# Kernel optimization log

Measured on AMD Instinct MI355X. Metric: run time of the kernel, lower is better.

Reference implementation:

```python
import jax, jax.numpy as jnp
import numpy as np

EPS = 1e-5
LEAK = 0.33  # scn LeakyReLU default leakiness


def leaky(x):
    return jnp.where(x > 0, x, LEAK * x)


def subm_conv(feat, idx, mask, w):
    # feat: [N,C], idx: [N,K] int, mask: [N,K] bool, w: [K,Cin,Cout]
    g = feat[idx] * mask[..., None]          # [N,K,C] gather of active neighbors
    return jnp.einsum('nkc,kcd->nd', g, w)   # [N,Cout]


def batch_norm(x, gamma, beta):
    # scn BatchNormalization in training mode: batch stats over active sites
    m = x.mean(axis=0)
    v = x.var(axis=0)
    return (x - m) * jax.lax.rsqrt(v + EPS) * gamma + beta


def setup_inputs() -> dict:
    key = jax.random.key(0)
    ks = jax.random.split(key, 8)
    N, K, C, B = 131072, 9, 64, 4
    features = jax.random.normal(ks[0], (N, C), dtype=jnp.float32)
    neighbor_idx = jax.random.randint(ks[1], (N, K), 0, N, dtype=jnp.int32)
    # center offset always points at self (submanifold conv semantics)
    neighbor_idx = neighbor_idx.at[:, K // 2].set(jnp.arange(N, dtype=jnp.int32))
    neighbor_mask = jax.random.randint(ks[2], (N, K), 0, 2) > 0
    neighbor_mask = neighbor_mask.at[:, K // 2].set(True)
    scale = 1.0 / np.sqrt(K * C)
    conv1_w = jax.random.normal(ks[3], (B, K, C, C), dtype=jnp.float32) * scale
    conv2_w = jax.random.normal(ks[4], (B, K, C, C), dtype=jnp.float32) * scale
    bn1_gamma = jnp.ones((B, C), dtype=jnp.float32)
    bn1_beta = jnp.zeros((B, C), dtype=jnp.float32)
    bn2_gamma = jnp.ones((B, C), dtype=jnp.float32)
    bn2_beta = jnp.zeros((B, C), dtype=jnp.float32)
    return {
        'features': features, 'neighbor_idx': neighbor_idx, 'neighbor_mask': neighbor_mask,
        'conv1_w': conv1_w, 'bn1_gamma': bn1_gamma, 'bn1_beta': bn1_beta,
        'conv2_w': conv2_w, 'bn2_gamma': bn2_gamma, 'bn2_beta': bn2_beta,
    }


def reference(features, neighbor_idx, neighbor_mask, conv1_w, bn1_gamma, bn1_beta,
              conv2_w, bn2_gamma, bn2_beta):
    x = features
    n_blocks = conv1_w.shape[0]
    for b in range(n_blocks):
        residual = x
        out = subm_conv(x, neighbor_idx, neighbor_mask, conv1_w[b])
        out = leaky(batch_norm(out, bn1_gamma[b], bn1_beta[b]))
        out = subm_conv(out, neighbor_idx, neighbor_mask, conv2_w[b])
        out = batch_norm(out, bn2_gamma[b], bn2_beta[b])
        x = leaky(out + residual)
    return x
```

## Files before the change

kernel.cpp:

```cpp
#include <hip/hip_runtime.h>
#include <hip/hip_bf16.h>
#include <stdint.h>

#define NROWS 131072
#define EPSBN 1e-5f
#define LEAKK 0.33f

typedef __bf16 bf16x8_t __attribute__((ext_vector_type(8)));
typedef float  f32x4_t  __attribute__((ext_vector_type(4)));

__device__ __forceinline__ float leaky_f(float x) { return fmaxf(x, LEAKK * x); }

#define GLDS16(g, l)                                                          \
    __builtin_amdgcn_global_load_lds(                                         \
        (const __attribute__((address_space(1))) void*)(g),                   \
        (__attribute__((address_space(3))) void*)(l), 16, 0, 0)

#define CFENCE() asm volatile("" ::: "memory")

__global__ __launch_bounds__(256, 2) void conv_kernel(
    const __bf16* __restrict__ src,
    const int* __restrict__ cidxT,
    const __bf16* __restrict__ wt,
    __bf16* __restrict__ dst,
    float* __restrict__ stat_out)
{
    __shared__ char Bw[9][8192];

    const int tid  = threadIdx.x;
    const int lane = tid & 63;
    const int wv   = tid >> 6;
    const int quad = lane >> 4;
    const int l15  = lane & 15;
    const int row0 = blockIdx.x << 8;
    const int srow = tid >> 3;
    const int cg   = (tid & 7) ^ (srow & 7);
    const int ldsl = (tid & 192) << 4;
    const int sxor = l15 & 7;

    const char* srcb = (const char*)src;
    const char* wtb  = (const char*)wt;

    f32x4_t acc[4][4];
#pragma unroll
    for (int mt = 0; mt < 4; ++mt)
#pragma unroll
        for (int nt = 0; nt < 4; ++nt)
            acc[mt][nt] = (f32x4_t){0.f, 0.f, 0.f, 0.f};

    const int ibase = row0 + (wv << 6) + l15;
    const unsigned qofs = (unsigned)(quad << 4);

    int ixv[2][4];
#pragma unroll
    for (int mt = 0; mt < 4; ++mt) ixv[0][mt] = cidxT[ibase + (mt << 4)];
#pragma unroll
    for (int mt = 0; mt < 4; ++mt) ixv[1][mt] = cidxT[NROWS + ibase + (mt << 4)];
    CFENCE();
#pragma unroll
    for (int k = 0; k < 9; ++k)
#pragma unroll
        for (int i = 0; i < 2; ++i)
            GLDS16(wtb + (k << 13) + (((i << 5) + srow) << 7) + (cg << 4),
                   &Bw[k][(i << 12) + ldsl]);
    CFENCE();
    asm volatile("s_waitcnt vmcnt(0)" ::: "memory");
    __builtin_amdgcn_s_barrier();
    CFENCE();

    bf16x8_t areg[2][4][2];
#pragma unroll
    for (int mt = 0; mt < 4; ++mt) {
        unsigned vo = ((unsigned)ixv[0][mt] << 7) + qofs;
#pragma unroll
        for (int ks = 0; ks < 2; ++ks)
            areg[0][mt][ks] = *(const bf16x8_t*)(srcb + vo + (ks << 6));
    }
    CFENCE();

#pragma unroll
    for (int k = 0; k < 9; ++k) {
        if (k < 7) {
#pragma unroll
            for (int mt = 0; mt < 4; ++mt)
                ixv[k & 1][mt] = cidxT[(k + 2) * NROWS + ibase + (mt << 4)];
        }
        if (k < 8) {
#pragma unroll
            for (int mt = 0; mt < 4; ++mt) {
                unsigned vo = ((unsigned)ixv[(k + 1) & 1][mt] << 7) + qofs;
#pragma unroll
                for (int ks = 0; ks < 2; ++ks)
                    areg[(k + 1) & 1][mt][ks] =
                        *(const bf16x8_t*)(srcb + vo + (ks << 6));
            }
        }
        CFENCE();
        bf16x8_t bq[4][2];
#pragma unroll
        for (int ks = 0; ks < 2; ++ks) {
            const int slot = ((quad | (ks << 2)) ^ sxor) << 4;
#pragma unroll
            for (int nt = 0; nt < 4; ++nt)
                bq[nt][ks] = *(const bf16x8_t*)
                    &Bw[k][(((nt << 4) + l15) << 7) + slot];
        }
#pragma unroll
        for (int ks = 0; ks < 2; ++ks)
#pragma unroll
            for (int mt = 0; mt < 4; ++mt)
#pragma unroll
                for (int nt = 0; nt < 4; ++nt)
                    acc[mt][nt] = __builtin_amdgcn_mfma_f32_16x16x32_bf16(
                        areg[k & 1][mt][ks], bq[nt][ks], acc[mt][nt], 0, 0, 0);
        CFENCE();
    }

#pragma unroll
    for (int mt = 0; mt < 4; ++mt) {
        int rowb = row0 + (wv << 6) + (mt << 4) + (quad << 2);
#pragma unroll
        for (int nt = 0; nt < 4; ++nt) {
            int col = (nt << 4) + l15;
#pragma unroll
            for (int r = 0; r < 4; ++r)
                dst[((size_t)(rowb + r) << 6) + col] = (__bf16)acc[mt][nt][r];
        }
    }
    float* red = (float*)Bw;
    __syncthreads();
    if (tid < 128) red[tid] = 0.f;
    __syncthreads();
#pragma unroll
    for (int nt = 0; nt < 4; ++nt) {
        float s = 0.f, q = 0.f;
#pragma unroll
        for (int mt = 0; mt < 4; ++mt)
#pragma unroll
            for (int r = 0; r < 4; ++r) { float v = acc[mt][nt][r]; s += v; q += v * v; }
        s += __shfl_xor(s, 16); s += __shfl_xor(s, 32);
        q += __shfl_xor(q, 16); q += __shfl_xor(q, 32);
        if (lane < 16) {
            atomicAdd(&red[(nt << 4) + lane], s);
            atomicAdd(&red[64 + (nt << 4) + lane], q);
        }
    }
    __syncthreads();
    if (tid < 128) atomicAdd(&stat_out[tid], red[tid]);
}

__global__ __launch_bounds__(256) void bnact_kernel(
    __bf16* __restrict__ y, const float* __restrict__ stat,
    const float* __restrict__ gamma, const float* __restrict__ beta)
{
    __shared__ float sc[64], sh[64];
    int tid = threadIdx.x;
    if (tid < 64) {
        float m = stat[tid] * (1.f / NROWS);
        float v = stat[64 + tid] * (1.f / NROWS) - m * m;
        float s = gamma[tid] * rsqrtf(v + EPSBN);
        sc[tid] = s;
        sh[tid] = beta[tid] - m * s;
    }
    __syncthreads();
    size_t base = ((((size_t)blockIdx.x << 8) | tid) << 3);
    int c0 = (int)(base & 63);
    bf16x8_t hv = *(bf16x8_t*)(y + base);
#pragma unroll
    for (int j = 0; j < 8; ++j) {
        float f = (float)hv[j];
        f = leaky_f(f * sc[c0 + j] + sh[c0 + j]);
        hv[j] = (__bf16)f;
    }
    *(bf16x8_t*)(y + base) = hv;
}

__global__ __launch_bounds__(256) void resid_kernel(
    const __bf16* __restrict__ z, const float* __restrict__ featin,
    __bf16* __restrict__ xh, float* __restrict__ dout,
    const float* __restrict__ stat, const float* __restrict__ gamma,
    const float* __restrict__ beta, int isfirst, int isfinal)
{
    __shared__ float sc[64], sh[64];
    int tid = threadIdx.x;
    if (tid < 64) {
        float m = stat[tid] * (1.f / NROWS);
        float v = stat[64 + tid] * (1.f / NROWS) - m * m;
        float s = gamma[tid] * rsqrtf(v + EPSBN);
        sc[tid] = s;
        sh[tid] = beta[tid] - m * s;
    }
    __syncthreads();
    size_t base = ((((size_t)blockIdx.x << 8) | tid) << 3);
    int c0 = (int)(base & 63);
    bf16x8_t zv = *(const bf16x8_t*)(z + base);
    float xv[8];
    if (isfirst) {
        float4 xa = *(const float4*)(featin + base);
        float4 xb = *(const float4*)(featin + base + 4);
#pragma unroll
        for (int j = 0; j < 4; ++j) { xv[j] = (&xa.x)[j]; xv[4 + j] = (&xb.x)[j]; }
    } else {
        bf16x8_t xr = *(const bf16x8_t*)(xh + base);
#pragma unroll
        for (int j = 0; j < 8; ++j) xv[j] = (float)xr[j];
    }
    float o[8];
#pragma unroll
    for (int j = 0; j < 8; ++j)
        o[j] = leaky_f((float)zv[j] * sc[c0 + j] + sh[c0 + j] + xv[j]);
    if (isfinal) {
        *(float4*)(dout + base)     = make_float4(o[0], o[1], o[2], o[3]);
        *(float4*)(dout + base + 4) = make_float4(o[4], o[5], o[6], o[7]);
    } else {
        bf16x8_t h;
#pragma unroll
        for (int j = 0; j < 8; ++j) h[j] = (__bf16)o[j];
        *(bf16x8_t*)(xh + base) = h;
    }
}

__global__ __launch_bounds__(256) void prep_kernel(
    const float* __restrict__ feat, const float* __restrict__ w1,
    const float* __restrict__ w2, const int* __restrict__ nidx,
    const unsigned char* __restrict__ mraw,
    __bf16* __restrict__ fh, __bf16* __restrict__ yh,
    __bf16* __restrict__ wtp, int* __restrict__ cidxT,
    float* __restrict__ stats)
{
    size_t t = ((size_t)blockIdx.x << 8) | threadIdx.x;
    if (t < 1024) stats[t] = 0.f;
    if (t < 64) {
        fh[(size_t)NROWS * 64 + t] = (__bf16)0.f;
        yh[(size_t)NROWS * 64 + t] = (__bf16)0.f;
    }
    if (t < 1048576) {
        size_t i = t << 3;
        float4 a = *(const float4*)(feat + i);
        float4 b = *(const float4*)(feat + i + 4);
        bf16x8_t h;
        h[0] = (__bf16)a.x; h[1] = (__bf16)a.y; h[2] = (__bf16)a.z; h[3] = (__bf16)a.w;
        h[4] = (__bf16)b.x; h[5] = (__bf16)b.y; h[6] = (__bf16)b.z; h[7] = (__bf16)b.w;
        *(bf16x8_t*)(fh + i) = h;
    }
    if (t < 294912) {
        int o = (int)t;
        int c = o & 63, d = (o >> 6) & 63;
        int kk = o >> 12;
        int k = kk % 9, bb = (kk / 9) & 3, cv = kk / 36;
        const float* w = cv ? w2 : w1;
        float v = w[((size_t)((bb * 9 + k) * 64 + c) << 6) + d];
        wtp[o] = (__bf16)v;
    }
    if (t < NROWS) {
        int n = (int)t;
        bool benc = (mraw[13] != 0);
        const unsigned int* mw = (const unsigned int*)mraw;
#pragma unroll
        for (int j = 0; j < 9; ++j) {
            int e = n * 9 + j;
            bool m = benc ? (mraw[e] != 0) : (mw[e] != 0u);
            cidxT[j * NROWS + n] = m ? nidx[e] : NROWS;
        }
    }
}

extern "C" void kernel_launch(void* const* d_in, const int* in_sizes, int n_in,
                              void* d_out, int out_size, void* d_ws, size_t ws_size,
                              hipStream_t stream) {
    const float* feat = (const float*)d_in[0];
    const int* nidx = (const int*)d_in[1];
    const unsigned char* mraw = (const unsigned char*)d_in[2];
    const float* w1 = (const float*)d_in[3];
    const float* g1 = (const float*)d_in[4];
    const float* b1 = (const float*)d_in[5];
    const float* w2 = (const float*)d_in[6];
    const float* g2 = (const float*)d_in[7];
    const float* b2 = (const float*)d_in[8];
    float* out = (float*)d_out;

    char* ws = (char*)d_ws;
    __bf16* xh    = (__bf16*)ws;
    __bf16* yh    = (__bf16*)(ws + 17825792);
    __bf16* zh    = (__bf16*)(ws + 35651584);
    __bf16* wtp   = (__bf16*)(ws + 53477376);
    float*  stats = (float*)(ws + 54525952);
    int*    cidxT = (int*)(ws + 54591488);

    prep_kernel<<<4096, 256, 0, stream>>>(feat, w1, w2, nidx, mraw,
                                          xh, yh, wtp, cidxT, stats);

    for (int b = 0; b < 4; ++b) {
        conv_kernel<<<512, 256, 0, stream>>>(
            xh, cidxT, wtp + (size_t)b * 9 * 4096,
            yh, stats + (size_t)(2 * b) * 128);
        bnact_kernel<<<4096, 256, 0, stream>>>(
            yh, stats + (size_t)(2 * b) * 128, g1 + b * 64, b1 + b * 64);
        conv_kernel<<<512, 256, 0, stream>>>(
            yh, cidxT, wtp + (size_t)(4 + b) * 9 * 4096,
            zh, stats + (size_t)(2 * b + 1) * 128);
        resid_kernel<<<4096, 256, 0, stream>>>(
            zh, feat, xh, out,
            stats + (size_t)(2 * b + 1) * 128, g2 + b * 64, b2 + b * 64,
            (b == 0) ? 1 : 0, (b == 3) ? 1 : 0);
    }
}
```

Baseline: 404.2 us.

## Fuse batch-norm, activation and residual into conv via a grid-wide barrier

The separate bnact and resid elementwise kernels are removed. Each conv launch now runs a fixed 256-block grid of 512 threads that accumulates BN statistics, waits at a software grid barrier (an atomic counter plus spin), and then applies normalisation, LeakyReLU and the optional residual directly to the accumulators before writing. This drops the intermediate bf16 tensor round-trips and half of the kernel launches per block. The gather prefetch is deepened to three stages and MFMA issue priority is raised with setprio. The barrier relies on all 256 blocks being co-resident and has a bounded spin that would silently give wrong stats on timeout.

```diff
diff --git a/kernel.cpp b/kernel.cpp
--- a/kernel.cpp
+++ b/kernel.cpp
@@ -5,6 +5,7 @@
 #define NROWS 131072
 #define EPSBN 1e-5f
 #define LEAKK 0.33f
+#define NBLK  256
 
 typedef __bf16 bf16x8_t __attribute__((ext_vector_type(8)));
 typedef float  f32x4_t  __attribute__((ext_vector_type(4)));
@@ -18,12 +19,15 @@
 
 #define CFENCE() asm volatile("" ::: "memory")
 
-__global__ __launch_bounds__(256, 2) void conv_kernel(
+__global__ __launch_bounds__(512, 1) void conv_kernel(
     const __bf16* __restrict__ src,
     const int* __restrict__ cidxT,
     const __bf16* __restrict__ wt,
-    __bf16* __restrict__ dst,
-    float* __restrict__ stat_out)
+    __bf16* dst,
+    float* __restrict__ stat,
+    const float* __restrict__ gamma, const float* __restrict__ beta,
+    const __bf16* residh, const float* residf,
+    float* dout, int mode)
 {
     __shared__ char Bw[9][8192];
 
@@ -32,10 +36,10 @@
     const int wv   = tid >> 6;
     const int quad = lane >> 4;
     const int l15  = lane & 15;
-    const int row0 = blockIdx.x << 8;
+    const int row0 = blockIdx.x << 9;
     const int srow = tid >> 3;
     const int cg   = (tid & 7) ^ (srow & 7);
-    const int ldsl = (tid & 192) << 4;
+    const int ldsl = (tid & 448) << 4;
     const int sxor = l15 & 7;
 
     const char* srcb = (const char*)src;
@@ -51,47 +55,49 @@
     const int ibase = row0 + (wv << 6) + l15;
     const unsigned qofs = (unsigned)(quad << 4);
 
-    int ixv[2][4];
-#pragma unroll
-    for (int mt = 0; mt < 4; ++mt) ixv[0][mt] = cidxT[ibase + (mt << 4)];
-#pragma unroll
-    for (int mt = 0; mt < 4; ++mt) ixv[1][mt] = cidxT[NROWS + ibase + (mt << 4)];
+#pragma unroll
+    for (int k = 0; k < 9; ++k)
+        GLDS16(wtb + (k << 13) + (srow << 7) + (cg << 4), &Bw[k][ldsl]);
     CFENCE();
-#pragma unroll
-    for (int k = 0; k < 9; ++k)
-#pragma unroll
-        for (int i = 0; i < 2; ++i)
-            GLDS16(wtb + (k << 13) + (((i << 5) + srow) << 7) + (cg << 4),
-                   &Bw[k][(i << 12) + ldsl]);
+    int ixv[3][4];
+#pragma unroll
+    for (int kk = 0; kk < 3; ++kk)
+#pragma unroll
+        for (int mt = 0; mt < 4; ++mt)
+            ixv[kk][mt] = cidxT[kk * NROWS + ibase + (mt << 4)];
     CFENCE();
-    asm volatile("s_waitcnt vmcnt(0)" ::: "memory");
+    asm volatile("s_waitcnt vmcnt(12)" ::: "memory");
     __builtin_amdgcn_s_barrier();
     CFENCE();
 
-    bf16x8_t areg[2][4][2];
-#pragma unroll
-    for (int mt = 0; mt < 4; ++mt) {
-        unsigned vo = ((unsigned)ixv[0][mt] << 7) + qofs;
-#pragma unroll
-        for (int ks = 0; ks < 2; ++ks)
-            areg[0][mt][ks] = *(const bf16x8_t*)(srcb + vo + (ks << 6));
-    }
-    CFENCE();
+    bf16x8_t areg[3][4][2];
+#pragma unroll
+    for (int kk = 0; kk < 2; ++kk) {
+#pragma unroll
+        for (int mt = 0; mt < 4; ++mt) {
+            unsigned vo = ((unsigned)ixv[kk][mt] << 7) + qofs;
+#pragma unroll
+            for (int ks = 0; ks < 2; ++ks)
+                areg[kk][mt][ks] = *(const bf16x8_t*)(srcb + vo + (ks << 6));
+        }
+        CFENCE();
+    }
 
 #pragma unroll
     for (int k = 0; k < 9; ++k) {
+        if (k < 6) {
+#pragma unroll
+            for (int mt = 0; mt < 4; ++mt)
+                ixv[k % 3][mt] = cidxT[(k + 3) * NROWS + ibase + (mt << 4)];
+        }
+        CFENCE();
         if (k < 7) {
 #pragma unroll
-            for (int mt = 0; mt < 4; ++mt)
-                ixv[k & 1][mt] = cidxT[(k + 2) * NROWS + ibase + (mt << 4)];
-        }
-        if (k < 8) {
-#pragma unroll
             for (int mt = 0; mt < 4; ++mt) {
-                unsigned vo = ((unsigned)ixv[(k + 1) & 1][mt] << 7) + qofs;
+                unsigned vo = ((unsigned)ixv[(k + 2) % 3][mt] << 7) + qofs;
 #pragma unroll
                 for (int ks = 0; ks < 2; ++ks)
-                    areg[(k + 1) & 1][mt][ks] =
+                    areg[(k + 2) % 3][mt][ks] =
                         *(const bf16x8_t*)(srcb + vo + (ks << 6));
             }
         }
@@ -105,6 +111,7 @@
                 bq[nt][ks] = *(const bf16x8_t*)
                     &Bw[k][(((nt << 4) + l15) << 7) + slot];
         }
+        __builtin_amdgcn_s_setprio(1);
 #pragma unroll
         for (int ks = 0; ks < 2; ++ks)
 #pragma unroll
@@ -112,22 +119,14 @@
 #pragma unroll
                 for (int nt = 0; nt < 4; ++nt)
                     acc[mt][nt] = __builtin_amdgcn_mfma_f32_16x16x32_bf16(
-                        areg[k & 1][mt][ks], bq[nt][ks], acc[mt][nt], 0, 0, 0);
-        CFENCE();
-    }
-
-#pragma unroll
-    for (int mt = 0; mt < 4; ++mt) {
-        int rowb = row0 + (wv << 6) + (mt << 4) + (quad << 2);
-#pragma unroll
-        for (int nt = 0; nt < 4; ++nt) {
-            int col = (nt << 4) + l15;
-#pragma unroll
-            for (int r = 0; r < 4; ++r)
-                dst[((size_t)(rowb + r) << 6) + col] = (__bf16)acc[mt][nt][r];
-        }
-    }
+                        areg[k % 3][mt][ks], bq[nt][ks], acc[mt][nt], 0, 0, 0);
+        __builtin_amdgcn_s_setprio(0);
+        CFENCE();
+    }
+
     float* red = (float*)Bw;
+    float* sc  = red + 128;
+    float* sh  = red + 192;
     __syncthreads();
     if (tid < 128) red[tid] = 0.f;
     __syncthreads();
@@ -146,77 +145,54 @@
         }
     }
     __syncthreads();
-    if (tid < 128) atomicAdd(&stat_out[tid], red[tid]);
-}
-
-__global__ __launch_bounds__(256) void bnact_kernel(
-    __bf16* __restrict__ y, const float* __restrict__ stat,
-    const float* __restrict__ gamma, const float* __restrict__ beta)
-{
-    __shared__ float sc[64], sh[64];
-    int tid = threadIdx.x;
+    if (tid < 128) atomicAdd(&stat[tid], red[tid]);
+    __threadfence();
+    __syncthreads();
+
+    int* cnt = (int*)(stat + 128);
+    if (tid == 0) {
+        __hip_atomic_fetch_add(cnt, 1, __ATOMIC_ACQ_REL, __HIP_MEMORY_SCOPE_AGENT);
+        int it = 0;
+        while (__hip_atomic_load(cnt, __ATOMIC_ACQUIRE, __HIP_MEMORY_SCOPE_AGENT)
+                   < NBLK && it < (1 << 20)) {
+            __builtin_amdgcn_s_sleep(2);
+            ++it;
+        }
+    }
+    __syncthreads();
+    __threadfence();
+
     if (tid < 64) {
-        float m = stat[tid] * (1.f / NROWS);
-        float v = stat[64 + tid] * (1.f / NROWS) - m * m;
+        float sm = __hip_atomic_load(&stat[tid],      __ATOMIC_ACQUIRE,
+                                     __HIP_MEMORY_SCOPE_AGENT);
+        float sq = __hip_atomic_load(&stat[64 + tid], __ATOMIC_ACQUIRE,
+                                     __HIP_MEMORY_SCOPE_AGENT);
+        float m = sm * (1.f / NROWS);
+        float v = sq * (1.f / NROWS) - m * m;
         float s = gamma[tid] * rsqrtf(v + EPSBN);
         sc[tid] = s;
         sh[tid] = beta[tid] - m * s;
     }
     __syncthreads();
-    size_t base = ((((size_t)blockIdx.x << 8) | tid) << 3);
-    int c0 = (int)(base & 63);
-    bf16x8_t hv = *(bf16x8_t*)(y + base);
-#pragma unroll
-    for (int j = 0; j < 8; ++j) {
-        float f = (float)hv[j];
-        f = leaky_f(f * sc[c0 + j] + sh[c0 + j]);
-        hv[j] = (__bf16)f;
-    }
-    *(bf16x8_t*)(y + base) = hv;
-}
-
-__global__ __launch_bounds__(256) void resid_kernel(
-    const __bf16* __restrict__ z, const float* __restrict__ featin,
-    __bf16* __restrict__ xh, float* __restrict__ dout,
-    const float* __restrict__ stat, const float* __restrict__ gamma,
-    const float* __restrict__ beta, int isfirst, int isfinal)
-{
-    __shared__ float sc[64], sh[64];
-    int tid = threadIdx.x;
-    if (tid < 64) {
-        float m = stat[tid] * (1.f / NROWS);
-        float v = stat[64 + tid] * (1.f / NROWS) - m * m;
-        float s = gamma[tid] * rsqrtf(v + EPSBN);
-        sc[tid] = s;
-        sh[tid] = beta[tid] - m * s;
-    }
-    __syncthreads();
-    size_t base = ((((size_t)blockIdx.x << 8) | tid) << 3);
-    int c0 = (int)(base & 63);
-    bf16x8_t zv = *(const bf16x8_t*)(z + base);
-    float xv[8];
-    if (isfirst) {
-        float4 xa = *(const float4*)(featin + base);
-        float4 xb = *(const float4*)(featin + base + 4);
-#pragma unroll
-        for (int j = 0; j < 4; ++j) { xv[j] = (&xa.x)[j]; xv[4 + j] = (&xb.x)[j]; }
-    } else {
-        bf16x8_t xr = *(const bf16x8_t*)(xh + base);
-#pragma unroll
-        for (int j = 0; j < 8; ++j) xv[j] = (float)xr[j];
-    }
-    float o[8];
-#pragma unroll
-    for (int j = 0; j < 8; ++j)
-        o[j] = leaky_f((float)zv[j] * sc[c0 + j] + sh[c0 + j] + xv[j]);
-    if (isfinal) {
-        *(float4*)(dout + base)     = make_float4(o[0], o[1], o[2], o[3]);
-        *(float4*)(dout + base + 4) = make_float4(o[4], o[5], o[6], o[7]);
-    } else {
-        bf16x8_t h;
-#pragma unroll
-        for (int j = 0; j < 8; ++j) h[j] = (__bf16)o[j];
-        *(bf16x8_t*)(xh + base) = h;
+
+#pragma unroll
+    for (int mt = 0; mt < 4; ++mt) {
+        int rowb = row0 + (wv << 6) + (mt << 4) + (quad << 2);
+#pragma unroll
+        for (int nt = 0; nt < 4; ++nt) {
+            int col = (nt << 4) + l15;
+            float scv = sc[col], shv = sh[col];
+#pragma unroll
+            for (int r = 0; r < 4; ++r) {
+                size_t off = ((size_t)(rowb + r) << 6) + col;
+                float v = acc[mt][nt][r] * scv + shv;
+                if (mode == 1 || mode == 3)      v += (float)residh[off];
+                else if (mode == 2)              v += residf[off];
+                v = leaky_f(v);
+                if (mode == 3) dout[off] = v;
+                else           dst[off]  = (__bf16)v;
+            }
+        }
     }
 }
 
@@ -229,7 +205,7 @@
     float* __restrict__ stats)
 {
     size_t t = ((size_t)blockIdx.x << 8) | threadIdx.x;
-    if (t < 1024) stats[t] = 0.f;
+    if (t < 2048) stats[t] = 0.f;
     if (t < 64) {
         fh[(size_t)NROWS * 64 + t] = (__bf16)0.f;
         yh[(size_t)NROWS * 64 + t] = (__bf16)0.f;
@@ -282,7 +258,6 @@
     char* ws = (char*)d_ws;
     __bf16* xh    = (__bf16*)ws;
     __bf16* yh    = (__bf16*)(ws + 17825792);
-    __bf16* zh    = (__bf16*)(ws + 35651584);
     __bf16* wtp   = (__bf16*)(ws + 53477376);
     float*  stats = (float*)(ws + 54525952);
     int*    cidxT = (int*)(ws + 54591488);
@@ -291,17 +266,15 @@
                                           xh, yh, wtp, cidxT, stats);
 
     for (int b = 0; b < 4; ++b) {
-        conv_kernel<<<512, 256, 0, stream>>>(
-            xh, cidxT, wtp + (size_t)b * 9 * 4096,
-            yh, stats + (size_t)(2 * b) * 128);
-        bnact_kernel<<<4096, 256, 0, stream>>>(
-            yh, stats + (size_t)(2 * b) * 128, g1 + b * 64, b1 + b * 64);
-        conv_kernel<<<512, 256, 0, stream>>>(
-            yh, cidxT, wtp + (size_t)(4 + b) * 9 * 4096,
-            zh, stats + (size_t)(2 * b + 1) * 128);
-        resid_kernel<<<4096, 256, 0, stream>>>(
-            zh, feat, xh, out,
-            stats + (size_t)(2 * b + 1) * 128, g2 + b * 64, b2 + b * 64,
-            (b == 0) ? 1 : 0, (b == 3) ? 1 : 0);
+        conv_kernel<<<NBLK, 512, 0, stream>>>(
+            xh, cidxT, wtp + (size_t)b * 9 * 4096, yh,
+            stats + (size_t)(2 * b) * 256, g1 + b * 64, b1 + b * 64,
+            nullptr, nullptr, nullptr, 0);
+        int mode = (b == 3) ? 3 : ((b == 0) ? 2 : 1);
+        conv_kernel<<<NBLK, 512, 0, stream>>>(
+            yh, cidxT, wtp + (size_t)(4 + b) * 9 * 4096, xh,
+            stats + (size_t)(2 * b + 1) * 256, g2 + b * 64, b2 + b * 64,
+            (b == 0) ? nullptr : xh, (b == 0) ? feat : nullptr,
+            (b == 3) ? out : nullptr, mode);
     }
 }
```

New measurement: 984.1 us. 2.43x slower.

## Double-buffer conv weights in LDS, halve rows per block, spread stat atomics

Applied to the files above, without the earlier changes.

The conv kernel no longer preloads all nine weight taps into LDS. It streams each tap into a two-slot LDS ring while the gather loads are issued, using explicit vmcnt waits and barriers. Each block now covers 128 rows instead of 256, which halves the accumulator and register footprint, raises the launch-bounds occupancy target to 4, and doubles the grid. BN statistic atomics are spread over 8 copies that the consumer kernels sum, to cut atomic contention. In exchange there are two extra barriers per tap and hand-tuned waitcnt values that must match the exact number of outstanding loads.

```diff
diff --git a/kernel.cpp b/kernel.cpp
--- a/kernel.cpp
+++ b/kernel.cpp
@@ -5,6 +5,7 @@
 #define NROWS 131072
 #define EPSBN 1e-5f
 #define LEAKK 0.33f
+#define NCOPY 8
 
 typedef __bf16 bf16x8_t __attribute__((ext_vector_type(8)));
 typedef float  f32x4_t  __attribute__((ext_vector_type(4)));
@@ -18,21 +19,21 @@
 
 #define CFENCE() asm volatile("" ::: "memory")
 
-__global__ __launch_bounds__(256, 2) void conv_kernel(
+__global__ __launch_bounds__(256, 4) void conv_kernel(
     const __bf16* __restrict__ src,
     const int* __restrict__ cidxT,
     const __bf16* __restrict__ wt,
     __bf16* __restrict__ dst,
     float* __restrict__ stat_out)
 {
-    __shared__ char Bw[9][8192];
+    __shared__ char Bw[2][8192];
 
     const int tid  = threadIdx.x;
     const int lane = tid & 63;
     const int wv   = tid >> 6;
     const int quad = lane >> 4;
     const int l15  = lane & 15;
-    const int row0 = blockIdx.x << 8;
+    const int row0 = blockIdx.x << 7;
     const int srow = tid >> 3;
     const int cg   = (tid & 7) ^ (srow & 7);
     const int ldsl = (tid & 192) << 4;
@@ -41,36 +42,30 @@
     const char* srcb = (const char*)src;
     const char* wtb  = (const char*)wt;
 
-    f32x4_t acc[4][4];
-#pragma unroll
-    for (int mt = 0; mt < 4; ++mt)
+    f32x4_t acc[2][4];
+#pragma unroll
+    for (int mt = 0; mt < 2; ++mt)
 #pragma unroll
         for (int nt = 0; nt < 4; ++nt)
             acc[mt][nt] = (f32x4_t){0.f, 0.f, 0.f, 0.f};
 
-    const int ibase = row0 + (wv << 6) + l15;
+    const int ibase = row0 + (wv << 5) + l15;
     const unsigned qofs = (unsigned)(quad << 4);
 
-    int ixv[2][4];
-#pragma unroll
-    for (int mt = 0; mt < 4; ++mt) ixv[0][mt] = cidxT[ibase + (mt << 4)];
-#pragma unroll
-    for (int mt = 0; mt < 4; ++mt) ixv[1][mt] = cidxT[NROWS + ibase + (mt << 4)];
+    int ixv[2][2];
+#pragma unroll
+    for (int mt = 0; mt < 2; ++mt) ixv[0][mt] = cidxT[ibase + (mt << 4)];
+#pragma unroll
+    for (int mt = 0; mt < 2; ++mt) ixv[1][mt] = cidxT[NROWS + ibase + (mt << 4)];
     CFENCE();
 #pragma unroll
-    for (int k = 0; k < 9; ++k)
-#pragma unroll
-        for (int i = 0; i < 2; ++i)
-            GLDS16(wtb + (k << 13) + (((i << 5) + srow) << 7) + (cg << 4),
-                   &Bw[k][(i << 12) + ldsl]);
+    for (int i = 0; i < 2; ++i)
+        GLDS16(wtb + (((i << 5) + srow) << 7) + (cg << 4),
+               &Bw[0][(i << 12) + ldsl]);
     CFENCE();
-    asm volatile("s_waitcnt vmcnt(0)" ::: "memory");
-    __builtin_amdgcn_s_barrier();
-    CFENCE();
-
-    bf16x8_t areg[2][4][2];
-#pragma unroll
-    for (int mt = 0; mt < 4; ++mt) {
+    bf16x8_t areg[2][2][2];
+#pragma unroll
+    for (int mt = 0; mt < 2; ++mt) {
         unsigned vo = ((unsigned)ixv[0][mt] << 7) + qofs;
 #pragma unroll
         for (int ks = 0; ks < 2; ++ks)
@@ -82,12 +77,21 @@
     for (int k = 0; k < 9; ++k) {
         if (k < 7) {
 #pragma unroll
-            for (int mt = 0; mt < 4; ++mt)
+            for (int mt = 0; mt < 2; ++mt)
                 ixv[k & 1][mt] = cidxT[(k + 2) * NROWS + ibase + (mt << 4)];
         }
+        CFENCE();
         if (k < 8) {
 #pragma unroll
-            for (int mt = 0; mt < 4; ++mt) {
+            for (int i = 0; i < 2; ++i)
+                GLDS16(wtb + ((size_t)(k + 1) << 13)
+                           + (((i << 5) + srow) << 7) + (cg << 4),
+                       &Bw[(k + 1) & 1][(i << 12) + ldsl]);
+        }
+        CFENCE();
+        if (k < 8) {
+#pragma unroll
+            for (int mt = 0; mt < 2; ++mt) {
                 unsigned vo = ((unsigned)ixv[(k + 1) & 1][mt] << 7) + qofs;
 #pragma unroll
                 for (int ks = 0; ks < 2; ++ks)
@@ -96,6 +100,10 @@
             }
         }
         CFENCE();
+        if (k < 7)       asm volatile("s_waitcnt vmcnt(12)" ::: "memory");
+        else if (k == 7) asm volatile("s_waitcnt vmcnt(10)" ::: "memory");
+        else             asm volatile("s_waitcnt vmcnt(4)"  ::: "memory");
+        __builtin_amdgcn_s_barrier();
         bf16x8_t bq[4][2];
 #pragma unroll
         for (int ks = 0; ks < 2; ++ks) {
@@ -103,22 +111,27 @@
 #pragma unroll
             for (int nt = 0; nt < 4; ++nt)
                 bq[nt][ks] = *(const bf16x8_t*)
-                    &Bw[k][(((nt << 4) + l15) << 7) + slot];
-        }
+                    &Bw[k & 1][(((nt << 4) + l15) << 7) + slot];
+        }
+        __builtin_amdgcn_s_setprio(1);
 #pragma unroll
         for (int ks = 0; ks < 2; ++ks)
 #pragma unroll
-            for (int mt = 0; mt < 4; ++mt)
+            for (int mt = 0; mt < 2; ++mt)
 #pragma unroll
                 for (int nt = 0; nt < 4; ++nt)
                     acc[mt][nt] = __builtin_amdgcn_mfma_f32_16x16x32_bf16(
                         areg[k & 1][mt][ks], bq[nt][ks], acc[mt][nt], 0, 0, 0);
-        CFENCE();
-    }
-
-#pragma unroll
-    for (int mt = 0; mt < 4; ++mt) {
-        int rowb = row0 + (wv << 6) + (mt << 4) + (quad << 2);
+        __builtin_amdgcn_s_setprio(0);
+        CFENCE();
+        asm volatile("s_waitcnt lgkmcnt(0)" ::: "memory");
+        __builtin_amdgcn_s_barrier();
+        CFENCE();
+    }
+
+#pragma unroll
+    for (int mt = 0; mt < 2; ++mt) {
+        int rowb = row0 + (wv << 5) + (mt << 4) + (quad << 2);
 #pragma unroll
         for (int nt = 0; nt < 4; ++nt) {
             int col = (nt << 4) + l15;
@@ -135,7 +148,7 @@
     for (int nt = 0; nt < 4; ++nt) {
         float s = 0.f, q = 0.f;
 #pragma unroll
-        for (int mt = 0; mt < 4; ++mt)
+        for (int mt = 0; mt < 2; ++mt)
 #pragma unroll
             for (int r = 0; r < 4; ++r) { float v = acc[mt][nt][r]; s += v; q += v * v; }
         s += __shfl_xor(s, 16); s += __shfl_xor(s, 32);
@@ -146,7 +159,8 @@
         }
     }
     __syncthreads();
-    if (tid < 128) atomicAdd(&stat_out[tid], red[tid]);
+    if (tid < 128)
+        atomicAdd(&stat_out[((blockIdx.x & (NCOPY - 1)) << 7) + tid], red[tid]);
 }
 
 __global__ __launch_bounds__(256) void bnact_kernel(
@@ -155,9 +169,18 @@
 {
     __shared__ float sc[64], sh[64];
     int tid = threadIdx.x;
+    if (tid < 128) {
+        float s = 0.f;
+#pragma unroll
+        for (int c = 0; c < NCOPY; ++c) s += stat[(c << 7) + tid];
+        ((float*)sc)[tid >= 64 ? 0 : 0] = 0.f;
+        if (tid < 64) sc[tid] = s;
+        else          sh[tid - 64] = s;
+    }
+    __syncthreads();
     if (tid < 64) {
-        float m = stat[tid] * (1.f / NROWS);
-        float v = stat[64 + tid] * (1.f / NROWS) - m * m;
+        float m = sc[tid] * (1.f / NROWS);
+        float v = sh[tid] * (1.f / NROWS) - m * m;
         float s = gamma[tid] * rsqrtf(v + EPSBN);
         sc[tid] = s;
         sh[tid] = beta[tid] - m * s;
@@ -183,9 +206,17 @@
 {
     __shared__ float sc[64], sh[64];
     int tid = threadIdx.x;
+    if (tid < 128) {
+        float s = 0.f;
+#pragma unroll
+        for (int c = 0; c < NCOPY; ++c) s += stat[(c << 7) + tid];
+        if (tid < 64) sc[tid] = s;
+        else          sh[tid - 64] = s;
+    }
+    __syncthreads();
     if (tid < 64) {
-        float m = stat[tid] * (1.f / NROWS);
-        float v = stat[64 + tid] * (1.f / NROWS) - m * m;
+        float m = sc[tid] * (1.f / NROWS);
+        float v = sh[tid] * (1.f / NROWS) - m * m;
         float s = gamma[tid] * rsqrtf(v + EPSBN);
         sc[tid] = s;
         sh[tid] = beta[tid] - m * s;
@@ -229,7 +260,7 @@
     float* __restrict__ stats)
 {
     size_t t = ((size_t)blockIdx.x << 8) | threadIdx.x;
-    if (t < 1024) stats[t] = 0.f;
+    if (t < 8192) stats[t] = 0.f;
     if (t < 64) {
         fh[(size_t)NROWS * 64 + t] = (__bf16)0.f;
         yh[(size_t)NROWS * 64 + t] = (__bf16)0.f;
@@ -291,17 +322,17 @@
                                           xh, yh, wtp, cidxT, stats);
 
     for (int b = 0; b < 4; ++b) {
-        conv_kernel<<<512, 256, 0, stream>>>(
+        conv_kernel<<<1024, 256, 0, stream>>>(
             xh, cidxT, wtp + (size_t)b * 9 * 4096,
-            yh, stats + (size_t)(2 * b) * 128);
+            yh, stats + (size_t)(2 * b) * 1024);
         bnact_kernel<<<4096, 256, 0, stream>>>(
-            yh, stats + (size_t)(2 * b) * 128, g1 + b * 64, b1 + b * 64);
-        conv_kernel<<<512, 256, 0, stream>>>(
+            yh, stats + (size_t)(2 * b) * 1024, g1 + b * 64, b1 + b * 64);
+        conv_kernel<<<1024, 256, 0, stream>>>(
             yh, cidxT, wtp + (size_t)(4 + b) * 9 * 4096,
-            zh, stats + (size_t)(2 * b + 1) * 128);
+            zh, stats + (size_t)(2 * b + 1) * 1024);
         resid_kernel<<<4096, 256, 0, stream>>>(
             zh, feat, xh, out,
-            stats + (size_t)(2 * b + 1) * 128, g2 + b * 64, b2 + b * 64,
+            stats + (size_t)(2 * b + 1) * 1024, g2 + b * 64, b2 + b * 64,
             (b == 0) ? 1 : 0, (b == 3) ? 1 : 0);
     }
 }
```

Measured after the change: 355.4 us. 1.14x faster.
